# Optimization experiments

Hardware: AMD Instinct MI355X
Metric: run time of the kernel (lower is better)

## Reference

```python
import jax, jax.numpy as jnp
import numpy as np

H = 10        # hidden size hardcoded in the torch module
MAX_PAD = 3   # static upper bound on zero_pad values (setup generates 0..2)
EPS = 1e-5    # torch BatchNorm1d default eps


def _batchnorm(x, gamma, beta):
    # training-mode BatchNorm1d: batch mean, biased batch variance
    m = jnp.mean(x, axis=0)
    v = jnp.var(x, axis=0)
    return (x - m) * jax.lax.rsqrt(v + EPS) * gamma + beta


def setup_inputs() -> dict:
    N, D = 65536, 512
    key = jax.random.key(0)
    ks = jax.random.split(key, 12)
    return {
        "x": jax.random.normal(ks[0], (N, D), jnp.float32),
        "zero_pad": jax.random.randint(ks[1], (N,), 0, MAX_PAD),
        "broad_id": jnp.sort(jax.random.randint(ks[2], (N,), 0, 8192)),
        "W1": jax.random.normal(ks[3], (H, D), jnp.float32) * 0.05,
        "b1": jax.random.normal(ks[4], (H,), jnp.float32) * 0.05,
        "g1": jnp.ones((H,), jnp.float32),
        "be1": jnp.zeros((H,), jnp.float32),
        "W_ih": jax.random.normal(ks[5], (4 * H, H), jnp.float32) * 0.2,
        "W_hh": jax.random.normal(ks[6], (4 * H, H), jnp.float32) * 0.2,
        "b_ih": jax.random.normal(ks[7], (4 * H,), jnp.float32) * 0.2,
        "b_hh": jax.random.normal(ks[8], (4 * H,), jnp.float32) * 0.2,
        "g2": jnp.ones((H,), jnp.float32),
        "be2": jnp.zeros((H,), jnp.float32),
        "W2": jax.random.normal(ks[9], (1, H), jnp.float32) * 0.3,
        "b2": jnp.zeros((1,), jnp.float32),
    }


def reference(x, zero_pad, broad_id, W1, b1, g1, be1, W_ih, W_hh, b_ih, b_hh, g2, be2, W2, b2):
    x1 = _batchnorm(x @ W1.T + b1, g1, be1)  # [N, H]
    # group boundary: last step of each broad_id run (incl. the final step)
    bnd = jnp.concatenate([broad_id[1:] != broad_id[:-1], jnp.array([True])])

    def cell(xin, h, c):
        g = xin @ W_ih.T + b_ih + h @ W_hh.T + b_hh  # [4H]
        i, f, gg, o = jnp.split(g, 4)                # torch gate order i,f,g,o
        i = jax.nn.sigmoid(i); f = jax.nn.sigmoid(f)
        gg = jnp.tanh(gg);     o = jax.nn.sigmoid(o)
        c2 = f * c + i * gg
        return o * jnp.tanh(c2), c2

    zin = jnp.zeros((H,), x1.dtype)

    def step(carry, inp):
        h, c, sh, sc, cnt = carry
        xi, zp, b = inp
        # dynamic zero-pad repeats, expressed as fixed-length masked loop
        for k in range(MAX_PAD):
            h2, c2 = cell(zin, h, c)
            m = k < zp
            h = jnp.where(m, h2, h)
            c = jnp.where(m, c2, c)
        ht, ct = cell(xi, h, c)
        # NOTE: within a group, (h, c) is NOT advanced by ht/ct -- faithful to source
        sh = sh + ht; sc = sc + ct; cnt = cnt + 1.0
        hn = jnp.where(b, sh / cnt, h)
        cn = jnp.where(b, sc / cnt, c)
        sh = jnp.where(b, 0.0, sh)
        sc = jnp.where(b, 0.0, sc)
        cnt = jnp.where(b, 0.0, cnt)
        return (hn, cn, sh, sc, cnt), ht

    z = jnp.zeros((H,), x1.dtype)
    init = (z, z, z, z, jnp.float32(0.0))
    _, outs = jax.lax.scan(step, init, (x1, zero_pad, bnd))  # outs: [N, H]
    out = _batchnorm(outs, g2, be2) @ W2.T + b2              # [N, 1]
    return jnp.tanh(out)
```

## Files before the change

kernel.cpp:

```cpp
#include <hip/hip_runtime.h>

#define NR 65536
#define DIN 512
#define H 10
#define G4 40
#define EPSB 1e-5f
#define CHUNK 32
#define WPB 4
#define WARM 32
#define SPW (WARM + CHUNK)
#define SLOTS (WARM + WPB*CHUNK)
#define NBLK (NR / (WPB * CHUNK))
#define RPB (WPB * CHUNK)
#define LOG2E 1.442695041f

__device__ __forceinline__ float fast_rcp(float x) {
  return __builtin_amdgcn_rcpf(x);
}
__device__ __forceinline__ float rlane(float v, int l) {
  return __int_as_float(__builtin_amdgcn_readlane(__float_as_int(v), l));
}
#define QP(v, code)                                                       \
  __int_as_float(__builtin_amdgcn_mov_dpp(__float_as_int(v), (code), 0xF, \
                                          0xF, true))
#define ROR(v, N)                                                          \
  __int_as_float(__builtin_amdgcn_mov_dpp(__float_as_int(v), 0x120 + (N), \
                                          0xF, 0xF, true))

__global__ __launch_bounds__(256) void k1_proj(const float* __restrict__ x,
                                               const float* __restrict__ W1,
                                               const float* __restrict__ b1,
                                               float* __restrict__ y,
                                               float* __restrict__ part1) {
  const int tid = threadIdx.x;
  const int lane = tid & 63;
  const int wv = tid >> 6;
  const int gw = blockIdx.x * 4 + wv;

  float w[H][8];
#pragma unroll
  for (int j = 0; j < H; ++j) {
    float4 a = *(const float4*)&W1[j * DIN + lane * 8];
    float4 b = *(const float4*)&W1[j * DIN + lane * 8 + 4];
    w[j][0] = a.x; w[j][1] = a.y; w[j][2] = a.z; w[j][3] = a.w;
    w[j][4] = b.x; w[j][5] = b.y; w[j][6] = b.z; w[j][7] = b.w;
  }
  const float bj = (lane < H) ? b1[lane] : 0.0f;
  float s1 = 0.0f, s2 = 0.0f;

  const int r0 = gw * 32;
  float4 xa = *(const float4*)&x[(size_t)r0 * DIN + lane * 8];
  float4 xb = *(const float4*)&x[(size_t)r0 * DIN + lane * 8 + 4];

  for (int i = 0; i < 32; ++i) {
    const int r = r0 + i;
    const int rn = (i + 1 < 32) ? r + 1 : r;
    float4 na = *(const float4*)&x[(size_t)rn * DIN + lane * 8];
    float4 nb = *(const float4*)&x[(size_t)rn * DIN + lane * 8 + 4];

    float acc[H];
#pragma unroll
    for (int j = 0; j < H; ++j) {
      float s = xa.x * w[j][0];
      s = fmaf(xa.y, w[j][1], s);
      s = fmaf(xa.z, w[j][2], s);
      s = fmaf(xa.w, w[j][3], s);
      s = fmaf(xb.x, w[j][4], s);
      s = fmaf(xb.y, w[j][5], s);
      s = fmaf(xb.z, w[j][6], s);
      s = fmaf(xb.w, w[j][7], s);
      acc[j] = s;
    }
#pragma unroll
    for (int j = 0; j < H; ++j) {
      float a = acc[j];
      a += ROR(a, 1);
      a += ROR(a, 2);
      a += ROR(a, 4);
      a += ROR(a, 8);
      acc[j] = a;
    }
    float tot[H];
#pragma unroll
    for (int j = 0; j < H; ++j) {
      float p0 = rlane(acc[j], 0);
      float p1 = rlane(acc[j], 16);
      float p2 = rlane(acc[j], 32);
      float p3 = rlane(acc[j], 48);
      tot[j] = (p0 + p1) + (p2 + p3);
    }
    float v = tot[0];
#pragma unroll
    for (int j = 1; j < H; ++j) v = (lane == j) ? tot[j] : v;
    if (lane < H) {
      v += bj;
      y[(size_t)r * H + lane] = v;
      s1 += v;
      s2 += v * v;
    }
    xa = na; xb = nb;
  }

  __shared__ float red[4][2 * H];
  if (lane < H) { red[wv][lane] = s1; red[wv][H + lane] = s2; }
  __syncthreads();
  if (tid < 2 * H) {
    float s = red[0][tid] + red[1][tid] + red[2][tid] + red[3][tid];
    part1[tid * NBLK + blockIdx.x] = s;
  }
}

__device__ __forceinline__ void cell40(float xin, float h, float c,
                                       const float (&w)[H], float bias,
                                       float As2, float Am, float Aa,
                                       float& ht, float& ct) {
  float a0 = bias + xin, a1 = 0.0f;
#pragma unroll
  for (int m = 0; m < H; m += 2) {
    float hm0 = rlane(h, 4 * m);
    float hm1 = rlane(h, 4 * (m + 1));
    a0 = fmaf(w[m], hm0, a0);
    a1 = fmaf(w[m + 1], hm1, a1);
  }
  float a = a0 + a1;
  float e = __builtin_amdgcn_exp2f(a * As2);
  float r = fast_rcp(1.0f + e);
  float gt = fmaf(r, Am, Aa);
  float gi = QP(gt, 0x00);
  float gf = QP(gt, 0x55);
  float gg = QP(gt, 0xAA);
  float go = QP(gt, 0xFF);
  ct = fmaf(gf, c, gi * gg);
  float e2 = __builtin_amdgcn_exp2f(ct * (-2.0f * LOG2E));
  float r2 = fast_rcp(1.0f + e2);
  float th = fmaf(r2, 2.0f, -1.0f);
  ht = go * th;
}

__global__ __launch_bounds__(256) void k3_scan(
    const float* __restrict__ y, const float* __restrict__ part1,
    const float* __restrict__ g1, const float* __restrict__ be1,
    const int* __restrict__ zp_arr, const int* __restrict__ broad,
    const float* __restrict__ Wih, const float* __restrict__ Whh,
    const float* __restrict__ bih, const float* __restrict__ bhh,
    float* __restrict__ outs, float* __restrict__ part2) {
  __shared__ __align__(16) float sxg[SLOTS * G4 + 64];
  __shared__ int szb[SLOTS];
  __shared__ float sy[SLOTS * H];
  __shared__ float wl[G4 * H];
  __shared__ float AB[2 * H];
  __shared__ float tot[2 * H];
  __shared__ float red[WPB][2 * H];

  const int tid = threadIdx.x;
  const int blk = blockIdx.x;
  const int lane = tid & 63;
  const int wv = tid >> 6;
  const int tw = blk * RPB - WARM;

  for (int j = wv; j < 2 * H; j += 4) {
    float s = 0.0f;
    for (int b = lane; b < NBLK; b += 64) s += part1[j * NBLK + b];
    s += ROR(s, 1); s += ROR(s, 2); s += ROR(s, 4); s += ROR(s, 8);
    float p0 = rlane(s, 0), p1 = rlane(s, 16);
    float p2 = rlane(s, 32), p3 = rlane(s, 48);
    if (lane == 0) tot[j] = (p0 + p1) + (p2 + p3);
  }
  for (int i = tid; i < SLOTS * H; i += 256) {
    const int slot = i / H;
    int t = tw + slot;
    t = t < 0 ? 0 : t;
    sy[i] = y[(size_t)t * H + (i - slot * H)];
  }
  for (int i = tid; i < G4 * H; i += 256) wl[i] = Wih[i];
  for (int i = tid; i < SLOTS; i += 256) {
    const int t = tw + i;
    const int tc = t < 0 ? 0 : t;
    const int z = zp_arr[tc];
    const int bn = (t + 1 >= NR) ? 1 : ((broad[tc + 1] != broad[tc]) ? 1 : 0);
    szb[i] = z | (bn << 8);
  }
  __syncthreads();

  if (tid < H) {
    float m = tot[tid] * (1.0f / NR);
    float v = tot[H + tid] * (1.0f / NR) - m * m;
    float inv = rsqrtf(v + EPSB);
    AB[tid] = inv * g1[tid];
    AB[H + tid] = be1[tid] - m * inv * g1[tid];
  }
  __syncthreads();

  if (tid < SLOTS) {
    float x1[H];
#pragma unroll
    for (int m = 0; m < H; ++m)
      x1[m] = fmaf(sy[tid * H + m], AB[m], AB[H + m]);
    float o[G4];
#pragma unroll
    for (int g = 0; g < 4; ++g) {
#pragma unroll
      for (int k = 0; k < H; ++k) {
        const int j = g * H + k;
        float s = 0.0f;
#pragma unroll
        for (int m = 0; m < H; ++m) s = fmaf(wl[j * H + m], x1[m], s);
        o[k * 4 + g] = s;
      }
    }
    float4* o4 = (float4*)&sxg[tid * G4];
#pragma unroll
    for (int q = 0; q < G4 / 4; ++q) o4[q] = ((const float4*)o)[q];
  }
  __syncthreads();

  if (lane < G4) {
    const int u = lane >> 2;
    const int g = lane & 3;

    const int row = g * H + u;
    float w[H];
#pragma unroll
    for (int m = 0; m < H; ++m) w[m] = Whh[row * H + m];
    const float bias = bih[row] + bhh[row];
    const bool isT = (g == 2);
    const float As2 = isT ? (-2.0f * LOG2E) : (-1.0f * LOG2E);
    const float Am = isT ? 2.0f : 1.0f;
    const float Aa = isT ? -1.0f : 0.0f;

    float h = 0.0f, c = 0.0f;
    float sh = 0.0f, sc = 0.0f, cntf = 0.0f;
    float s1 = 0.0f, s2 = 0.0f;

    const int slot0 = wv * CHUNK;
    float xv = sxg[slot0 * G4 + lane];
    int zb = szb[slot0];

    for (int s = 0; s < SPW; ++s) {
      const int slot = slot0 + s;
      const int slotn = (s + 1 < SPW) ? slot + 1 : slot;
      float xn = sxg[slotn * G4 + lane];
      int zbn = szb[slotn];

      const int t = tw + slot;
      if (t >= 0) {
        const int zbu = __builtin_amdgcn_readfirstlane(zb);
        const int zp = zbu & 0xFF;
        for (int p = 0; p < zp; ++p) {
          float h2, c2;
          cell40(0.0f, h, c, w, bias, As2, Am, Aa, h2, c2);
          h = h2; c = c2;
        }
        float ht, ct;
        cell40(xv, h, c, w, bias, As2, Am, Aa, ht, ct);
        sh += ht; sc += ct; cntf += 1.0f;

        if (s >= WARM) {
          if (g == 0) outs[(size_t)t * H + u] = ht;
          s1 += ht;
          s2 += ht * ht;
        }
        if (zbu & 256) {
          const float r = fast_rcp(cntf);
          h = sh * r; c = sc * r;
          sh = 0.0f; sc = 0.0f; cntf = 0.0f;
        }
      }
      xv = xn;
      zb = zbn;
    }
    if (g == 0) {
      red[wv][u] = s1;
      red[wv][H + u] = s2;
    }
  }
  __syncthreads();
  if (tid < 2 * H) {
    float s = red[0][tid] + red[1][tid] + red[2][tid] + red[3][tid];
    part2[tid * NBLK + blk] = s;
  }
}

__global__ __launch_bounds__(256) void k5_out(const float* __restrict__ part2,
                                              const float* __restrict__ g2,
                                              const float* __restrict__ be2,
                                              const float* __restrict__ W2,
                                              const float* __restrict__ b2,
                                              const float* __restrict__ outs,
                                              float* __restrict__ out) {
  __shared__ float tot[2 * H];
  __shared__ float contrib[H];
  __shared__ float cbs[H + 1];
  const int tid = threadIdx.x;
  const int lane = tid & 63;
  const int wv = tid >> 6;
  for (int j = wv; j < 2 * H; j += 4) {
    float s = 0.0f;
    for (int b = lane; b < NBLK; b += 64) s += part2[j * NBLK + b];
    s += ROR(s, 1); s += ROR(s, 2); s += ROR(s, 4); s += ROR(s, 8);
    float p0 = rlane(s, 0), p1 = rlane(s, 16);
    float p2 = rlane(s, 32), p3 = rlane(s, 48);
    if (lane == 0) tot[j] = (p0 + p1) + (p2 + p3);
  }
  __syncthreads();
  if (tid < H) {
    float m = tot[tid] * (1.0f / NR);
    float v = tot[H + tid] * (1.0f / NR) - m * m;
    float inv = rsqrtf(v + EPSB);
    cbs[tid] = inv * g2[tid] * W2[tid];
    contrib[tid] = (be2[tid] - m * inv * g2[tid]) * W2[tid];
  }
  __syncthreads();
  if (tid == 0) {
    float bacc = b2[0];
#pragma unroll
    for (int j = 0; j < H; ++j) bacc += contrib[j];
    cbs[H] = bacc;
  }
  __syncthreads();
  const int t = blockIdx.x * 256 + tid;
  float s = cbs[H];
  const float* r = outs + (size_t)t * H;
#pragma unroll
  for (int j = 0; j < H; ++j) s = fmaf(r[j], cbs[j], s);
  out[t] =
      1.0f - 2.0f * fast_rcp(__builtin_amdgcn_exp2f(2.0f * LOG2E * s) + 1.0f);
}

extern "C" void kernel_launch(void* const* d_in, const int* in_sizes, int n_in,
                              void* d_out, int out_size, void* d_ws,
                              size_t ws_size, hipStream_t stream) {
  const float* x = (const float*)d_in[0];
  const int* zp = (const int*)d_in[1];
  const int* broad = (const int*)d_in[2];
  const float* W1 = (const float*)d_in[3];
  const float* b1 = (const float*)d_in[4];
  const float* g1 = (const float*)d_in[5];
  const float* be1 = (const float*)d_in[6];
  const float* Wih = (const float*)d_in[7];
  const float* Whh = (const float*)d_in[8];
  const float* bih = (const float*)d_in[9];
  const float* bhh = (const float*)d_in[10];
  const float* g2 = (const float*)d_in[11];
  const float* be2 = (const float*)d_in[12];
  const float* W2 = (const float*)d_in[13];
  const float* b2 = (const float*)d_in[14];
  float* out = (float*)d_out;

  float* ws = (float*)d_ws;
  float* part1 = ws;
  float* part2 = ws + 2 * H * NBLK;
  float* y = ws + 4 * H * NBLK;
  float* outs = y + (size_t)NR * H;

  k1_proj<<<dim3(512), dim3(256), 0, stream>>>(x, W1, b1, y, part1);
  k3_scan<<<dim3(NBLK), dim3(256), 0, stream>>>(y, part1, g1, be1, zp, broad,
                                                Wih, Whh, bih, bhh, outs,
                                                part2);
  k5_out<<<dim3(NR / 256), dim3(256), 0, stream>>>(part2, g2, be2, W2, b2,
                                                   outs, out);
  (void)in_sizes; (void)n_in; (void)out_size; (void)ws_size;
}
```

Before: 274.1 us.

## Halve scan chunk size, deepen x prefetch, vectorize y staging, split input gates

Shrinks the per-wave scan chunk from 32 to 16 rows, doubling the scan grid to 1024 blocks so each block's sequential recurrence is shorter, while the 32-step warm-up overhead becomes relatively larger. The projection kernel now prefetches x two rows ahead instead of one to hide load latency. The scan kernel stages y with float4 copies for non-first blocks and spreads the input-gate precompute over two threads per slot. Partial-sum arrays are resized separately for the two kernels' block counts.

```diff
diff --git a/kernel.cpp b/kernel.cpp
--- a/kernel.cpp
+++ b/kernel.cpp
@@ -5,13 +5,14 @@
 #define H 10
 #define G4 40
 #define EPSB 1e-5f
-#define CHUNK 32
+#define CHUNK 16
 #define WPB 4
 #define WARM 32
 #define SPW (WARM + CHUNK)
 #define SLOTS (WARM + WPB*CHUNK)
-#define NBLK (NR / (WPB * CHUNK))
 #define RPB (WPB * CHUNK)
+#define NB1 512
+#define NB3 (NR / RPB)
 #define LOG2E 1.442695041f
 
 __device__ __forceinline__ float fast_rcp(float x) {
@@ -51,12 +52,14 @@
   const int r0 = gw * 32;
   float4 xa = *(const float4*)&x[(size_t)r0 * DIN + lane * 8];
   float4 xb = *(const float4*)&x[(size_t)r0 * DIN + lane * 8 + 4];
+  float4 ya = *(const float4*)&x[(size_t)(r0 + 1) * DIN + lane * 8];
+  float4 yb = *(const float4*)&x[(size_t)(r0 + 1) * DIN + lane * 8 + 4];
 
   for (int i = 0; i < 32; ++i) {
     const int r = r0 + i;
-    const int rn = (i + 1 < 32) ? r + 1 : r;
-    float4 na = *(const float4*)&x[(size_t)rn * DIN + lane * 8];
-    float4 nb = *(const float4*)&x[(size_t)rn * DIN + lane * 8 + 4];
+    const int rn = r0 + ((i + 2 < 32) ? i + 2 : 31);
+    float4 za = *(const float4*)&x[(size_t)rn * DIN + lane * 8];
+    float4 zb = *(const float4*)&x[(size_t)rn * DIN + lane * 8 + 4];
 
     float acc[H];
 #pragma unroll
@@ -98,7 +101,8 @@
       s1 += v;
       s2 += v * v;
     }
-    xa = na; xb = nb;
+    xa = ya; xb = yb;
+    ya = za; yb = zb;
   }
 
   __shared__ float red[4][2 * H];
@@ -106,7 +110,7 @@
   __syncthreads();
   if (tid < 2 * H) {
     float s = red[0][tid] + red[1][tid] + red[2][tid] + red[3][tid];
-    part1[tid * NBLK + blockIdx.x] = s;
+    part1[tid * NB1 + blockIdx.x] = s;
   }
 }
 
@@ -146,7 +150,7 @@
     float* __restrict__ outs, float* __restrict__ part2) {
   __shared__ __align__(16) float sxg[SLOTS * G4 + 64];
   __shared__ int szb[SLOTS];
-  __shared__ float sy[SLOTS * H];
+  __shared__ __align__(16) float sy[SLOTS * H];
   __shared__ float wl[G4 * H];
   __shared__ float AB[2 * H];
   __shared__ float tot[2 * H];
@@ -160,17 +164,22 @@
 
   for (int j = wv; j < 2 * H; j += 4) {
     float s = 0.0f;
-    for (int b = lane; b < NBLK; b += 64) s += part1[j * NBLK + b];
+    for (int b = lane; b < NB1; b += 64) s += part1[j * NB1 + b];
     s += ROR(s, 1); s += ROR(s, 2); s += ROR(s, 4); s += ROR(s, 8);
     float p0 = rlane(s, 0), p1 = rlane(s, 16);
     float p2 = rlane(s, 32), p3 = rlane(s, 48);
     if (lane == 0) tot[j] = (p0 + p1) + (p2 + p3);
   }
-  for (int i = tid; i < SLOTS * H; i += 256) {
-    const int slot = i / H;
-    int t = tw + slot;
-    t = t < 0 ? 0 : t;
-    sy[i] = y[(size_t)t * H + (i - slot * H)];
+  if (blk > 0) {
+    const float4* src = (const float4*)(y + (size_t)tw * H);
+    for (int i = tid; i < SLOTS * H / 4; i += 256) ((float4*)sy)[i] = src[i];
+  } else {
+    for (int i = tid; i < SLOTS * H; i += 256) {
+      const int slot = i / H;
+      int t = tw + slot;
+      t = t < 0 ? 0 : t;
+      sy[i] = y[(size_t)t * H + (i - slot * H)];
+    }
   }
   for (int i = tid; i < G4 * H; i += 256) wl[i] = Wih[i];
   for (int i = tid; i < SLOTS; i += 256) {
@@ -191,26 +200,25 @@
   }
   __syncthreads();
 
-  if (tid < SLOTS) {
+  if (tid < SLOTS * 2) {
+    const int slot = tid >> 1;
+    const int half = tid & 1;
     float x1[H];
 #pragma unroll
     for (int m = 0; m < H; ++m)
-      x1[m] = fmaf(sy[tid * H + m], AB[m], AB[H + m]);
-    float o[G4];
-#pragma unroll
-    for (int g = 0; g < 4; ++g) {
-#pragma unroll
-      for (int k = 0; k < H; ++k) {
-        const int j = g * H + k;
-        float s = 0.0f;
-#pragma unroll
-        for (int m = 0; m < H; ++m) s = fmaf(wl[j * H + m], x1[m], s);
-        o[k * 4 + g] = s;
+      x1[m] = fmaf(sy[slot * H + m], AB[m], AB[H + m]);
+#pragma unroll
+    for (int k = 0; k < H; ++k) {
+      const int j0 = (half * 2) * H + k;
+      const int j1 = (half * 2 + 1) * H + k;
+      float s0 = 0.0f, s1 = 0.0f;
+#pragma unroll
+      for (int m = 0; m < H; ++m) {
+        s0 = fmaf(wl[j0 * H + m], x1[m], s0);
+        s1 = fmaf(wl[j1 * H + m], x1[m], s1);
       }
-    }
-    float4* o4 = (float4*)&sxg[tid * G4];
-#pragma unroll
-    for (int q = 0; q < G4 / 4; ++q) o4[q] = ((const float4*)o)[q];
+      *(float2*)&sxg[slot * G4 + k * 4 + half * 2] = make_float2(s0, s1);
+    }
   }
   __syncthreads();
 
@@ -277,7 +285,7 @@
   __syncthreads();
   if (tid < 2 * H) {
     float s = red[0][tid] + red[1][tid] + red[2][tid] + red[3][tid];
-    part2[tid * NBLK + blk] = s;
+    part2[tid * NB3 + blk] = s;
   }
 }
 
@@ -296,7 +304,7 @@
   const int wv = tid >> 6;
   for (int j = wv; j < 2 * H; j += 4) {
     float s = 0.0f;
-    for (int b = lane; b < NBLK; b += 64) s += part2[j * NBLK + b];
+    for (int b = lane; b < NB3; b += 64) s += part2[j * NB3 + b];
     s += ROR(s, 1); s += ROR(s, 2); s += ROR(s, 4); s += ROR(s, 8);
     float p0 = rlane(s, 0), p1 = rlane(s, 16);
     float p2 = rlane(s, 32), p3 = rlane(s, 48);
@@ -349,14 +357,14 @@
 
   float* ws = (float*)d_ws;
   float* part1 = ws;
-  float* part2 = ws + 2 * H * NBLK;
-  float* y = ws + 4 * H * NBLK;
+  float* part2 = ws + 2 * H * NB1;
+  float* y = part2 + 2 * H * NB3;
   float* outs = y + (size_t)NR * H;
 
-  k1_proj<<<dim3(512), dim3(256), 0, stream>>>(x, W1, b1, y, part1);
-  k3_scan<<<dim3(NBLK), dim3(256), 0, stream>>>(y, part1, g1, be1, zp, broad,
-                                                Wih, Whh, bih, bhh, outs,
-                                                part2);
+  k1_proj<<<dim3(NB1), dim3(256), 0, stream>>>(x, W1, b1, y, part1);
+  k3_scan<<<dim3(NB3), dim3(256), 0, stream>>>(y, part1, g1, be1, zp, broad,
+                                               Wih, Whh, bih, bhh, outs,
+                                               part2);
   k5_out<<<dim3(NR / 256), dim3(256), 0, stream>>>(part2, g2, be2, W2, b2,
                                                    outs, out);
   (void)in_sizes; (void)n_in; (void)out_size; (void)ws_size;
```

Result: slower. 290.5 us (+6.0%).
